# Optimization experiments

Hardware: AMD Instinct MI355X
Metric: run time of the kernel (lower is better)

Reference implementation:

```python
import jax, jax.numpy as jnp
import numpy as np

B, T, C, H = 2, 2048, 1024, 16
HD = C // H  # head dim = 64


def setup_inputs() -> dict:
    key = jax.random.key(0)
    ks = jax.random.split(key, 5)
    s = 1.0 / np.sqrt(C)
    return {
        "x": jax.random.normal(ks[0], (B, T, C), dtype=jnp.float32),
        "W_attn": jax.random.normal(ks[1], (3 * C, C), dtype=jnp.float32) * s,
        "b_attn": jax.random.normal(ks[2], (3 * C,), dtype=jnp.float32) * 0.02,
        "W_proj": jax.random.normal(ks[3], (C, C), dtype=jnp.float32) * s,
        "b_proj": jax.random.normal(ks[4], (C,), dtype=jnp.float32) * 0.02,
    }


def reference(x, W_attn, b_attn, W_proj, b_proj):
    Bx, Tx, Cx = x.shape
    # fused QKV projection (torch Linear: x @ W.T + b)
    qkv = x @ W_attn.T + b_attn                      # [B,T,3C]
    q, k, v = jnp.split(qkv, 3, axis=-1)
    # [B,T,C] -> [B,H,T,hd]
    q = q.reshape(Bx, Tx, H, HD).transpose(0, 2, 1, 3)
    k = k.reshape(Bx, Tx, H, HD).transpose(0, 2, 1, 3)
    v = v.reshape(Bx, Tx, H, HD).transpose(0, 2, 1, 3)
    scale = 1.0 / np.sqrt(HD)
    att = jnp.einsum('bhqd,bhkd->bhqk', q, k) * scale  # [B,H,T,T]
    causal = jnp.tril(jnp.ones((Tx, Tx), dtype=bool))
    att = jnp.where(causal[None, None], att, -jnp.inf)
    att = jax.nn.softmax(att, axis=-1)
    y = jnp.einsum('bhqk,bhkd->bhqd', att, v)          # [B,H,T,hd]
    y = y.transpose(0, 2, 1, 3).reshape(Bx, Tx, Cx)
    return y @ W_proj.T + b_proj
```

## Files before the change

### kernel.cpp

```cpp
#include <hip/hip_runtime.h>

typedef unsigned short ushort_t;
typedef __bf16 bf16x8 __attribute__((ext_vector_type(8)));
typedef float f32x4 __attribute__((ext_vector_type(4)));

__device__ inline ushort_t f2bf(float f) {
  unsigned int u = __builtin_bit_cast(unsigned int, f);
  u += 0x7fff + ((u >> 16) & 1);
  return (ushort_t)(u >> 16);
}

__device__ inline unsigned pk_bf(float a, float b) {
  unsigned ua = __builtin_bit_cast(unsigned, a);
  unsigned ub = __builtin_bit_cast(unsigned, b);
  ua += 0x7fff + ((ua >> 16) & 1);
  ub += 0x7fff + ((ub >> 16) & 1);
  return __builtin_amdgcn_perm(ub, ua, 0x07060302);
}

__device__ inline void async_ld16(const ushort_t* g, const ushort_t* l) {
  __builtin_amdgcn_global_load_lds(
      (const __attribute__((address_space(1))) void*)g,
      (__attribute__((address_space(3))) void*)l, 16, 0, 0);
}

template <int IMM>
__device__ inline void waitcnt_barrier() {
  asm volatile("" ::: "memory");
  __builtin_amdgcn_s_waitcnt(IMM);
  __builtin_amdgcn_s_barrier();
  asm volatile("" ::: "memory");
}

__global__ void cvt_all(const float* __restrict__ x, const float* __restrict__ wa,
                        const float* __restrict__ wp, ushort_t* __restrict__ xb,
                        ushort_t* __restrict__ wab, ushort_t* __restrict__ wpb) {
  int i = blockIdx.x * 256 + threadIdx.x;
  const float* src;
  ushort_t* dst;
  int off;
  if (i < 1048576) { src = x; dst = xb; off = i; }
  else if (i < 1835008) { src = wa; dst = wab; off = i - 1048576; }
  else { src = wp; dst = wpb; off = i - 1835008; }
  float4 f = ((const float4*)src)[off];
  unsigned long long p = (unsigned long long)f2bf(f.x)
      | ((unsigned long long)f2bf(f.y) << 16)
      | ((unsigned long long)f2bf(f.z) << 32)
      | ((unsigned long long)f2bf(f.w) << 48);
  ((unsigned long long*)dst)[off] = p;
}

template <int BM, int BN, int IM, int JN, int MODE>
__global__ __launch_bounds__(256) void gemm_bt(
    const ushort_t* __restrict__ A, const ushort_t* __restrict__ B,
    const float* __restrict__ bias, float* __restrict__ Cf,
    ushort_t* __restrict__ Cb, ushort_t* __restrict__ vtb,
    int M, int N, int K, int ldc, float qscale) {
  constexpr int NWN = BN / (JN * 16);
  constexpr int NL = (BM + BN) / 64;
  constexpr int WIMM = 0x0F70 | NL;
  __shared__ __align__(16) ushort_t As[3][BM * 32];
  __shared__ __align__(16) ushort_t Bs[3][BN * 32];
  const int tid = threadIdx.x;
  const int wave = tid >> 6, lane = tid & 63;
  const int quad = lane >> 4, l16 = lane & 15;
  const int wr = wave / NWN, wc = wave % NWN;
  const int wm = wr * IM * 16, wn = wc * JN * 16;
  const int m0 = blockIdx.y * BM, n0 = blockIdx.x * BN;
  const ushort_t* Ag = A + (size_t)m0 * K;
  const ushort_t* Bg = B + (size_t)n0 * K;
  const int slot = (quad ^ ((l16 >> 1) & 3)) * 8;
  f32x4 acc[IM][JN] = {};

  auto stage = [&](int kt, int bsel) {
    int k0 = kt * 32;
#pragma unroll
    for (int p = 0; p < BM / 64; ++p) {
      int ci = p * 256 + tid;
      int row = ci >> 2, ch = (ci & 3) ^ ((ci >> 3) & 3);
      async_ld16(Ag + (size_t)row * K + k0 + ch * 8, As[bsel] + (p * 256 + wave * 64) * 8);
    }
#pragma unroll
    for (int p = 0; p < BN / 64; ++p) {
      int ci = p * 256 + tid;
      int row = ci >> 2, ch = (ci & 3) ^ ((ci >> 3) & 3);
      async_ld16(Bg + (size_t)row * K + k0 + ch * 8, Bs[bsel] + (p * 256 + wave * 64) * 8);
    }
  };

  const int KT = K / 32;
  stage(0, 0);
  stage(1, 1);
  for (int kt = 0; kt < KT; ++kt) {
    waitcnt_barrier<WIMM>();
    if (kt + 2 < KT) stage(kt + 2, (kt + 2) % 3);
    const ushort_t* Ac = As[kt % 3];
    const ushort_t* Bc = Bs[kt % 3];
    bf16x8 af[IM], bfr[JN];
#pragma unroll
    for (int i = 0; i < IM; ++i)
      af[i] = *(const bf16x8*)(Ac + (wm + i * 16 + l16) * 32 + slot);
#pragma unroll
    for (int j = 0; j < JN; ++j)
      bfr[j] = *(const bf16x8*)(Bc + (wn + j * 16 + l16) * 32 + slot);
#pragma unroll
    for (int i = 0; i < IM; ++i)
#pragma unroll
      for (int j = 0; j < JN; ++j)
        acc[i][j] = __builtin_amdgcn_mfma_f32_16x16x32_bf16(af[i], bfr[j], acc[i][j], 0, 0, 0);
  }

  if (MODE == 1 && n0 >= 2048) {
#pragma unroll
    for (int j = 0; j < JN; ++j) {
      int col = n0 + wn + j * 16 + l16;
      int cv = col - 2048;
      float bv = bias[col];
      size_t rowbase = ((size_t)(cv >> 6)) * 64 + (cv & 63);
#pragma unroll
      for (int i = 0; i < IM; ++i) {
        int rowb = m0 + wm + i * 16 + quad * 4;
        int bb = rowb >> 11, t = rowb & 2047;
        uint2 pp;
        pp.x = pk_bf(acc[i][j][0] + bv, acc[i][j][1] + bv);
        pp.y = pk_bf(acc[i][j][2] + bv, acc[i][j][3] + bv);
        *(uint2*)(vtb + (((size_t)bb * 1024 + rowbase) * 2048 + t)) = pp;
      }
    }
    return;
  }
#pragma unroll
  for (int j = 0; j < JN; ++j) {
    int col = n0 + wn + j * 16 + l16;
    float bv = bias[col];
    float sc = (MODE == 1 && col < 1024) ? qscale : 1.0f;
#pragma unroll
    for (int i = 0; i < IM; ++i)
#pragma unroll
      for (int r = 0; r < 4; ++r) {
        int row = m0 + wm + i * 16 + quad * 4 + r;
        float v = (acc[i][j][r] + bv) * sc;
        if (MODE == 1)
          Cb[(size_t)row * ldc + col] = f2bf(v);
        else
          Cf[(size_t)row * ldc + col] = v;
      }
  }
}

__global__ __launch_bounds__(256) void flash2(
    const ushort_t* __restrict__ qk, const ushort_t* __restrict__ vt,
    ushort_t* __restrict__ y) {
  __shared__ __align__(16) ushort_t Kb[3][4096];
  __shared__ __align__(16) ushort_t Vb[3][4096];
  __shared__ __align__(16) ushort_t Qa[4096], Qb[4096];
  __shared__ __align__(16) ushort_t Ps[64 * 72];
  const int tid = threadIdx.x, wave = tid >> 6, lane = tid & 63;
  const int quad = lane >> 4, l16 = lane & 15;
  const int r7 = l16 & 7;
  const int p = blockIdx.x, bh = blockIdx.y;
  const int b = bh >> 4, h = bh & 15;
  const int bT = b * 2048;
  const int qtA = 31 - p, qtB = p;

  auto stage = [&](int kt, int bsel) {
    int k0 = kt * 64;
#pragma unroll
    for (int i = 0; i < 2; ++i) {
      int ci = i * 256 + tid;
      int row = ci >> 3, ch = (ci & 7) ^ (row & 7);
      async_ld16(qk + (size_t)(bT + k0 + row) * 2048 + 1024 + h * 64 + ch * 8,
                 Kb[bsel] + (i * 256 + wave * 64) * 8);
      async_ld16(vt + (size_t)(bh * 64 + row) * 2048 + k0 + ch * 8,
                 Vb[bsel] + (i * 256 + wave * 64) * 8);
    }
  };

#pragma unroll
  for (int i = 0; i < 2; ++i) {
    int ci = i * 256 + tid;
    int row = ci >> 3, ch = (ci & 7) ^ (row & 7);
    async_ld16(qk + (size_t)(bT + qtA * 64 + row) * 2048 + h * 64 + ch * 8,
               Qa + (i * 256 + wave * 64) * 8);
    async_ld16(qk + (size_t)(bT + qtB * 64 + row) * 2048 + h * 64 + ch * 8,
               Qb + (i * 256 + wave * 64) * 8);
  }
  stage(0, 0);
  stage(1, 1);
  waitcnt_barrier<0x0F78>();
  bf16x8 qaA[2], qaB[2];
#pragma unroll
  for (int ks = 0; ks < 2; ++ks) {
    int off = (wave * 16 + l16) * 64 + (((ks * 4 + quad) ^ r7) * 8);
    qaA[ks] = *(const bf16x8*)(Qa + off);
    qaB[ks] = *(const bf16x8*)(Qb + off);
  }

  f32x4 oA[4] = {}, oB[4] = {};
  float lA = 0.f, lB = 0.f;

  auto process = [&](const bf16x8* qa, f32x4* o, float& l, bool diag,
                     const ushort_t* Kc, const ushort_t* Vc) {
    f32x4 s[4] = {};
#pragma unroll
    for (int ks = 0; ks < 2; ++ks) {
      bf16x8 qf = qa[ks];
#pragma unroll
      for (int j = 0; j < 4; ++j) {
        bf16x8 kf = *(const bf16x8*)(Kc + (j * 16 + l16) * 64 + (((ks * 4 + quad) ^ r7) * 8));
        s[j] = __builtin_amdgcn_mfma_f32_16x16x32_bf16(kf, qf, s[j], 0, 0, 0);
      }
    }
    if (diag) {
      int qloc = wave * 16 + l16;
#pragma unroll
      for (int j = 0; j < 4; ++j)
#pragma unroll
        for (int r = 0; r < 4; ++r)
          if (j * 16 + quad * 4 + r > qloc) s[j][r] = -1e30f;
    }
    float rs = 0.f;
#pragma unroll
    for (int j = 0; j < 4; ++j)
#pragma unroll
      for (int r = 0; r < 4; ++r) {
        float pv = exp2f(s[j][r]);
        s[j][r] = pv;
        rs += pv;
      }
    rs += __shfl_xor(rs, 16, 64);
    rs += __shfl_xor(rs, 32, 64);
    l += rs;
#pragma unroll
    for (int j = 0; j < 4; ++j) {
      uint2 pp;
      pp.x = pk_bf(s[j][0], s[j][1]);
      pp.y = pk_bf(s[j][2], s[j][3]);
      *(uint2*)(Ps + (wave * 16 + l16) * 72 + j * 16 + quad * 4) = pp;
    }
    __builtin_amdgcn_s_waitcnt(0xc07f);
#pragma unroll
    for (int ks = 0; ks < 2; ++ks) {
      bf16x8 pf = *(const bf16x8*)(Ps + (wave * 16 + l16) * 72 + ks * 32 + quad * 8);
#pragma unroll
      for (int j = 0; j < 4; ++j) {
        bf16x8 vf = *(const bf16x8*)(Vc + (j * 16 + l16) * 64 + (((ks * 4 + quad) ^ r7) * 8));
        o[j] = __builtin_amdgcn_mfma_f32_16x16x32_bf16(vf, pf, o[j], 0, 0, 0);
      }
    }
  };

  const int KT = qtA + 1;
  for (int kt = 0; kt < KT; ++kt) {
    waitcnt_barrier<0x0F74>();
    if (kt + 2 < KT) stage(kt + 2, (kt + 2) % 3);
    const ushort_t* Kc = Kb[kt % 3];
    const ushort_t* Vc = Vb[kt % 3];
    process(qaA, oA, lA, kt == qtA, Kc, Vc);
    if (kt <= qtB) process(qaB, oB, lB, kt == qtB, Kc, Vc);
  }

  auto wrt = [&](int qt, f32x4* o, float l) {
    float inv = 1.f / l;
    size_t row = (size_t)(bT + qt * 64 + wave * 16 + l16);
#pragma unroll
    for (int j = 0; j < 4; ++j) {
      uint2 pp;
      pp.x = pk_bf(o[j][0] * inv, o[j][1] * inv);
      pp.y = pk_bf(o[j][2] * inv, o[j][3] * inv);
      *(uint2*)(y + row * 1024 + h * 64 + j * 16 + quad * 4) = pp;
    }
  };
  wrt(qtA, oA, lA);
  wrt(qtB, oB, lB);
}

extern "C" void kernel_launch(void* const* d_in, const int* in_sizes, int n_in,
                              void* d_out, int out_size, void* d_ws, size_t ws_size,
                              hipStream_t stream) {
  const float* x  = (const float*)d_in[0];
  const float* Wa = (const float*)d_in[1];
  const float* ba = (const float*)d_in[2];
  const float* Wp = (const float*)d_in[3];
  const float* bp = (const float*)d_in[4];
  float* out = (float*)d_out;
  char* ws = (char*)d_ws;
  ushort_t* xb  = (ushort_t*)(ws);
  ushort_t* Wab = (ushort_t*)(ws + 8388608);
  ushort_t* Wpb = (ushort_t*)(ws + 14680064);
  ushort_t* qkb = (ushort_t*)(ws + 16777216);
  ushort_t* yb  = (ushort_t*)(ws + 33554432);
  ushort_t* vtb = (ushort_t*)(ws + 41943040);

  cvt_all<<<8192, 256, 0, stream>>>(x, Wa, Wp, xb, Wab, Wpb);
  gemm_bt<128, 128, 4, 4, 1><<<dim3(24, 32), 256, 0, stream>>>(
      xb, Wab, ba, nullptr, qkb, vtb, 4096, 3072, 1024, 2048, 0.18033688011112042f);
  flash2<<<dim3(16, 32), 256, 0, stream>>>(qkb, vtb, yb);
  gemm_bt<64, 64, 2, 2, 0><<<dim3(16, 64), 256, 0, stream>>>(
      yb, Wpb, bp, out, nullptr, nullptr, 4096, 1024, 1024, 1024, 1.0f);
}
```

Before: 202.3 us.

## Replace LDS-staged paired-tile flash attention with direct-load one-tile-per-block kernel

The attention kernel no longer stages K/V tiles through triple-buffered shared memory with barriers. Each wave now loads its K and V fragments straight from global memory into registers, and each block handles one query tile instead of a balanced pair, launching twice as many blocks. The goal is to remove barrier and LDS traffic and raise occupancy through much smaller shared memory use. In exchange, the four waves each reload the same K/V from global or L2, and the causal workload is now unbalanced across blocks.

Result: slower. 377.3 us (+86.5%).

```diff
diff --git a/kernel.cpp b/kernel.cpp
--- a/kernel.cpp
+++ b/kernel.cpp
@@ -148,70 +148,57 @@
   }
 }
 
-__global__ __launch_bounds__(256) void flash2(
+__global__ __launch_bounds__(256) void flash3(
     const ushort_t* __restrict__ qk, const ushort_t* __restrict__ vt,
     ushort_t* __restrict__ y) {
-  __shared__ __align__(16) ushort_t Kb[3][4096];
-  __shared__ __align__(16) ushort_t Vb[3][4096];
-  __shared__ __align__(16) ushort_t Qa[4096], Qb[4096];
-  __shared__ __align__(16) ushort_t Ps[64 * 72];
+  __shared__ __align__(16) ushort_t Ps[4][16 * 72];
   const int tid = threadIdx.x, wave = tid >> 6, lane = tid & 63;
   const int quad = lane >> 4, l16 = lane & 15;
-  const int r7 = l16 & 7;
-  const int p = blockIdx.x, bh = blockIdx.y;
+  const int qt = 31 - blockIdx.x;
+  const int bh = blockIdx.y;
   const int b = bh >> 4, h = bh & 15;
   const int bT = b * 2048;
-  const int qtA = 31 - p, qtB = p;
-
-  auto stage = [&](int kt, int bsel) {
-    int k0 = kt * 64;
-#pragma unroll
-    for (int i = 0; i < 2; ++i) {
-      int ci = i * 256 + tid;
-      int row = ci >> 3, ch = (ci & 7) ^ (row & 7);
-      async_ld16(qk + (size_t)(bT + k0 + row) * 2048 + 1024 + h * 64 + ch * 8,
-                 Kb[bsel] + (i * 256 + wave * 64) * 8);
-      async_ld16(vt + (size_t)(bh * 64 + row) * 2048 + k0 + ch * 8,
-                 Vb[bsel] + (i * 256 + wave * 64) * 8);
-    }
-  };
-
-#pragma unroll
-  for (int i = 0; i < 2; ++i) {
-    int ci = i * 256 + tid;
-    int row = ci >> 3, ch = (ci & 7) ^ (row & 7);
-    async_ld16(qk + (size_t)(bT + qtA * 64 + row) * 2048 + h * 64 + ch * 8,
-               Qa + (i * 256 + wave * 64) * 8);
-    async_ld16(qk + (size_t)(bT + qtB * 64 + row) * 2048 + h * 64 + ch * 8,
-               Qb + (i * 256 + wave * 64) * 8);
-  }
-  stage(0, 0);
-  stage(1, 1);
-  waitcnt_barrier<0x0F78>();
-  bf16x8 qaA[2], qaB[2];
-#pragma unroll
-  for (int ks = 0; ks < 2; ++ks) {
-    int off = (wave * 16 + l16) * 64 + (((ks * 4 + quad) ^ r7) * 8);
-    qaA[ks] = *(const bf16x8*)(Qa + off);
-    qaB[ks] = *(const bf16x8*)(Qb + off);
-  }
-
-  f32x4 oA[4] = {}, oB[4] = {};
-  float lA = 0.f, lB = 0.f;
-
-  auto process = [&](const bf16x8* qa, f32x4* o, float& l, bool diag,
-                     const ushort_t* Kc, const ushort_t* Vc) {
+  const int q0 = qt * 64;
+  ushort_t* Pw = Ps[wave];
+
+  const ushort_t* qrow = qk + (size_t)(bT + q0 + wave * 16 + l16) * 2048 + h * 64 + quad * 8;
+  bf16x8 qf[2];
+  qf[0] = *(const bf16x8*)(qrow);
+  qf[1] = *(const bf16x8*)(qrow + 32);
+
+  const ushort_t* kp[4];
+  const ushort_t* vp[4];
+#pragma unroll
+  for (int j = 0; j < 4; ++j) {
+    kp[j] = qk + (size_t)(bT + j * 16 + l16) * 2048 + 1024 + h * 64 + quad * 8;
+    vp[j] = vt + (size_t)(bh * 64 + j * 16 + l16) * 2048 + quad * 8;
+  }
+
+  f32x4 o[4] = {};
+  float lacc = 0.f;
+
+  for (int kt = 0; kt <= qt; ++kt) {
+    bf16x8 kf[4][2];
+#pragma unroll
+    for (int j = 0; j < 4; ++j) {
+      kf[j][0] = *(const bf16x8*)(kp[j]);
+      kf[j][1] = *(const bf16x8*)(kp[j] + 32);
+    }
     f32x4 s[4] = {};
 #pragma unroll
-    for (int ks = 0; ks < 2; ++ks) {
-      bf16x8 qf = qa[ks];
-#pragma unroll
-      for (int j = 0; j < 4; ++j) {
-        bf16x8 kf = *(const bf16x8*)(Kc + (j * 16 + l16) * 64 + (((ks * 4 + quad) ^ r7) * 8));
-        s[j] = __builtin_amdgcn_mfma_f32_16x16x32_bf16(kf, qf, s[j], 0, 0, 0);
-      }
-    }
-    if (diag) {
+    for (int ks = 0; ks < 2; ++ks)
+#pragma unroll
+      for (int j = 0; j < 4; ++j)
+        s[j] = __builtin_amdgcn_mfma_f32_16x16x32_bf16(kf[j][ks], qf[ks], s[j], 0, 0, 0);
+    bf16x8 vf[4][2];
+#pragma unroll
+    for (int j = 0; j < 4; ++j) {
+      vf[j][0] = *(const bf16x8*)(vp[j]);
+      vf[j][1] = *(const bf16x8*)(vp[j] + 32);
+      kp[j] += 64 * 2048;
+      vp[j] += 64;
+    }
+    if (kt == qt) {
       int qloc = wave * 16 + l16;
 #pragma unroll
       for (int j = 0; j < 4; ++j)
@@ -219,60 +206,43 @@
         for (int r = 0; r < 4; ++r)
           if (j * 16 + quad * 4 + r > qloc) s[j][r] = -1e30f;
     }
-    float rs = 0.f;
 #pragma unroll
     for (int j = 0; j < 4; ++j)
 #pragma unroll
       for (int r = 0; r < 4; ++r) {
         float pv = exp2f(s[j][r]);
         s[j][r] = pv;
-        rs += pv;
+        lacc += pv;
       }
-    rs += __shfl_xor(rs, 16, 64);
-    rs += __shfl_xor(rs, 32, 64);
-    l += rs;
 #pragma unroll
     for (int j = 0; j < 4; ++j) {
       uint2 pp;
       pp.x = pk_bf(s[j][0], s[j][1]);
       pp.y = pk_bf(s[j][2], s[j][3]);
-      *(uint2*)(Ps + (wave * 16 + l16) * 72 + j * 16 + quad * 4) = pp;
+      *(uint2*)(Pw + l16 * 72 + j * 16 + quad * 4) = pp;
     }
     __builtin_amdgcn_s_waitcnt(0xc07f);
-#pragma unroll
-    for (int ks = 0; ks < 2; ++ks) {
-      bf16x8 pf = *(const bf16x8*)(Ps + (wave * 16 + l16) * 72 + ks * 32 + quad * 8);
-#pragma unroll
-      for (int j = 0; j < 4; ++j) {
-        bf16x8 vf = *(const bf16x8*)(Vc + (j * 16 + l16) * 64 + (((ks * 4 + quad) ^ r7) * 8));
-        o[j] = __builtin_amdgcn_mfma_f32_16x16x32_bf16(vf, pf, o[j], 0, 0, 0);
-      }
-    }
-  };
-
-  const int KT = qtA + 1;
-  for (int kt = 0; kt < KT; ++kt) {
-    waitcnt_barrier<0x0F74>();
-    if (kt + 2 < KT) stage(kt + 2, (kt + 2) % 3);
-    const ushort_t* Kc = Kb[kt % 3];
-    const ushort_t* Vc = Vb[kt % 3];
-    process(qaA, oA, lA, kt == qtA, Kc, Vc);
-    if (kt <= qtB) process(qaB, oB, lB, kt == qtB, Kc, Vc);
-  }
-
-  auto wrt = [&](int qt, f32x4* o, float l) {
-    float inv = 1.f / l;
-    size_t row = (size_t)(bT + qt * 64 + wave * 16 + l16);
-#pragma unroll
-    for (int j = 0; j < 4; ++j) {
-      uint2 pp;
-      pp.x = pk_bf(o[j][0] * inv, o[j][1] * inv);
-      pp.y = pk_bf(o[j][2] * inv, o[j][3] * inv);
-      *(uint2*)(y + row * 1024 + h * 64 + j * 16 + quad * 4) = pp;
-    }
-  };
-  wrt(qtA, oA, lA);
-  wrt(qtB, oB, lB);
+    bf16x8 pf[2];
+    pf[0] = *(const bf16x8*)(Pw + l16 * 72 + quad * 8);
+    pf[1] = *(const bf16x8*)(Pw + l16 * 72 + 32 + quad * 8);
+#pragma unroll
+    for (int ks = 0; ks < 2; ++ks)
+#pragma unroll
+      for (int j = 0; j < 4; ++j)
+        o[j] = __builtin_amdgcn_mfma_f32_16x16x32_bf16(vf[j][ks], pf[ks], o[j], 0, 0, 0);
+  }
+
+  lacc += __shfl_xor(lacc, 16, 64);
+  lacc += __shfl_xor(lacc, 32, 64);
+  float inv = 1.f / lacc;
+  size_t row = (size_t)(bT + q0 + wave * 16 + l16);
+#pragma unroll
+  for (int j = 0; j < 4; ++j) {
+    uint2 pp;
+    pp.x = pk_bf(o[j][0] * inv, o[j][1] * inv);
+    pp.y = pk_bf(o[j][2] * inv, o[j][3] * inv);
+    *(uint2*)(y + row * 1024 + h * 64 + j * 16 + quad * 4) = pp;
+  }
 }
 
 extern "C" void kernel_launch(void* const* d_in, const int* in_sizes, int n_in,
@@ -295,7 +265,7 @@
   cvt_all<<<8192, 256, 0, stream>>>(x, Wa, Wp, xb, Wab, Wpb);
   gemm_bt<128, 128, 4, 4, 1><<<dim3(24, 32), 256, 0, stream>>>(
       xb, Wab, ba, nullptr, qkb, vtb, 4096, 3072, 1024, 2048, 0.18033688011112042f);
-  flash2<<<dim3(16, 32), 256, 0, stream>>>(qkb, vtb, yb);
+  flash3<<<dim3(32, 32), 256, 0, stream>>>(qkb, vtb, yb);
   gemm_bt<64, 64, 2, 2, 0><<<dim3(16, 64), 256, 0, stream>>>(
       yb, Wpb, bp, out, nullptr, nullptr, 4096, 1024, 1024, 1024, 1.0f);
 }
```

## Use 8-wave QKV GEMM and interleave two query tiles in flash kernel

Applied to the files above, without the earlier changes.

The QKV GEMM becomes a 512-thread, 8-wave kernel with each wave holding a 4x2 tile instead of 4x4, and the staging loops are generalized to the thread count. The flash kernel loads K fragments once per step and reuses them for both query tiles, gives each tile its own per-wave P buffer, and interleaves the two tiles' MFMAs. It also defers the cross-lane row-sum reduction to the final write. The aim is more latency hiding and fewer redundant LDS reads, at the cost of higher register pressure and possible occupancy loss.

New measurement: 239.2 us. 1.18x slower.

```diff
diff --git a/kernel.cpp b/kernel.cpp
--- a/kernel.cpp
+++ b/kernel.cpp
@@ -50,14 +50,14 @@
   ((unsigned long long*)dst)[off] = p;
 }
 
-template <int BM, int BN, int IM, int JN, int MODE>
-__global__ __launch_bounds__(256) void gemm_bt(
+template <int BM, int BN, int IM, int JN, int MODE, int TPB>
+__global__ __launch_bounds__(TPB) void gemm_bt(
     const ushort_t* __restrict__ A, const ushort_t* __restrict__ B,
     const float* __restrict__ bias, float* __restrict__ Cf,
     ushort_t* __restrict__ Cb, ushort_t* __restrict__ vtb,
     int M, int N, int K, int ldc, float qscale) {
   constexpr int NWN = BN / (JN * 16);
-  constexpr int NL = (BM + BN) / 64;
+  constexpr int NL = (BM + BN) * 32 / (TPB * 8);
   constexpr int WIMM = 0x0F70 | NL;
   __shared__ __align__(16) ushort_t As[3][BM * 32];
   __shared__ __align__(16) ushort_t Bs[3][BN * 32];
@@ -75,16 +75,16 @@
   auto stage = [&](int kt, int bsel) {
     int k0 = kt * 32;
 #pragma unroll
-    for (int p = 0; p < BM / 64; ++p) {
-      int ci = p * 256 + tid;
+    for (int p = 0; p < BM * 4 / TPB; ++p) {
+      int ci = p * TPB + tid;
       int row = ci >> 2, ch = (ci & 3) ^ ((ci >> 3) & 3);
-      async_ld16(Ag + (size_t)row * K + k0 + ch * 8, As[bsel] + (p * 256 + wave * 64) * 8);
-    }
-#pragma unroll
-    for (int p = 0; p < BN / 64; ++p) {
-      int ci = p * 256 + tid;
+      async_ld16(Ag + (size_t)row * K + k0 + ch * 8, As[bsel] + (p * TPB + wave * 64) * 8);
+    }
+#pragma unroll
+    for (int p = 0; p < BN * 4 / TPB; ++p) {
+      int ci = p * TPB + tid;
       int row = ci >> 2, ch = (ci & 3) ^ ((ci >> 3) & 3);
-      async_ld16(Bg + (size_t)row * K + k0 + ch * 8, Bs[bsel] + (p * 256 + wave * 64) * 8);
+      async_ld16(Bg + (size_t)row * K + k0 + ch * 8, Bs[bsel] + (p * TPB + wave * 64) * 8);
     }
   };
 
@@ -148,13 +148,13 @@
   }
 }
 
-__global__ __launch_bounds__(256) void flash2(
+__global__ __launch_bounds__(256) void flash4(
     const ushort_t* __restrict__ qk, const ushort_t* __restrict__ vt,
     ushort_t* __restrict__ y) {
   __shared__ __align__(16) ushort_t Kb[3][4096];
   __shared__ __align__(16) ushort_t Vb[3][4096];
   __shared__ __align__(16) ushort_t Qa[4096], Qb[4096];
-  __shared__ __align__(16) ushort_t Ps[64 * 72];
+  __shared__ __align__(16) ushort_t Ps[8][16 * 72];
   const int tid = threadIdx.x, wave = tid >> 6, lane = tid & 63;
   const int quad = lane >> 4, l16 = lane & 15;
   const int r7 = l16 & 7;
@@ -162,6 +162,8 @@
   const int b = bh >> 4, h = bh & 15;
   const int bT = b * 2048;
   const int qtA = 31 - p, qtB = p;
+  ushort_t* PwA = Ps[wave];
+  ushort_t* PwB = Ps[wave + 4];
 
   auto stage = [&](int kt, int bsel) {
     int k0 = kt * 64;
@@ -188,67 +190,16 @@
   stage(0, 0);
   stage(1, 1);
   waitcnt_barrier<0x0F78>();
-  bf16x8 qaA[2], qaB[2];
+  bf16x8 qfA[2], qfB[2];
 #pragma unroll
   for (int ks = 0; ks < 2; ++ks) {
     int off = (wave * 16 + l16) * 64 + (((ks * 4 + quad) ^ r7) * 8);
-    qaA[ks] = *(const bf16x8*)(Qa + off);
-    qaB[ks] = *(const bf16x8*)(Qb + off);
+    qfA[ks] = *(const bf16x8*)(Qa + off);
+    qfB[ks] = *(const bf16x8*)(Qb + off);
   }
 
   f32x4 oA[4] = {}, oB[4] = {};
   float lA = 0.f, lB = 0.f;
-
-  auto process = [&](const bf16x8* qa, f32x4* o, float& l, bool diag,
-                     const ushort_t* Kc, const ushort_t* Vc) {
-    f32x4 s[4] = {};
-#pragma unroll
-    for (int ks = 0; ks < 2; ++ks) {
-      bf16x8 qf = qa[ks];
-#pragma unroll
-      for (int j = 0; j < 4; ++j) {
-        bf16x8 kf = *(const bf16x8*)(Kc + (j * 16 + l16) * 64 + (((ks * 4 + quad) ^ r7) * 8));
-        s[j] = __builtin_amdgcn_mfma_f32_16x16x32_bf16(kf, qf, s[j], 0, 0, 0);
-      }
-    }
-    if (diag) {
-      int qloc = wave * 16 + l16;
-#pragma unroll
-      for (int j = 0; j < 4; ++j)
-#pragma unroll
-        for (int r = 0; r < 4; ++r)
-          if (j * 16 + quad * 4 + r > qloc) s[j][r] = -1e30f;
-    }
-    float rs = 0.f;
-#pragma unroll
-    for (int j = 0; j < 4; ++j)
-#pragma unroll
-      for (int r = 0; r < 4; ++r) {
-        float pv = exp2f(s[j][r]);
-        s[j][r] = pv;
-        rs += pv;
-      }
-    rs += __shfl_xor(rs, 16, 64);
-    rs += __shfl_xor(rs, 32, 64);
-    l += rs;
-#pragma unroll
-    for (int j = 0; j < 4; ++j) {
-      uint2 pp;
-      pp.x = pk_bf(s[j][0], s[j][1]);
-      pp.y = pk_bf(s[j][2], s[j][3]);
-      *(uint2*)(Ps + (wave * 16 + l16) * 72 + j * 16 + quad * 4) = pp;
-    }
-    __builtin_amdgcn_s_waitcnt(0xc07f);
-#pragma unroll
-    for (int ks = 0; ks < 2; ++ks) {
-      bf16x8 pf = *(const bf16x8*)(Ps + (wave * 16 + l16) * 72 + ks * 32 + quad * 8);
-#pragma unroll
-      for (int j = 0; j < 4; ++j) {
-        bf16x8 vf = *(const bf16x8*)(Vc + (j * 16 + l16) * 64 + (((ks * 4 + quad) ^ r7) * 8));
-        o[j] = __builtin_amdgcn_mfma_f32_16x16x32_bf16(vf, pf, o[j], 0, 0, 0);
-      }
-    }
-  };
 
   const int KT = qtA + 1;
   for (int kt = 0; kt < KT; ++kt) {
@@ -256,11 +207,87 @@
     if (kt + 2 < KT) stage(kt + 2, (kt + 2) % 3);
     const ushort_t* Kc = Kb[kt % 3];
     const ushort_t* Vc = Vb[kt % 3];
-    process(qaA, oA, lA, kt == qtA, Kc, Vc);
-    if (kt <= qtB) process(qaB, oB, lB, kt == qtB, Kc, Vc);
+    const bool doB = (kt <= qtB);
+
+    bf16x8 kf[4][2];
+#pragma unroll
+    for (int j = 0; j < 4; ++j)
+#pragma unroll
+      for (int ks = 0; ks < 2; ++ks)
+        kf[j][ks] = *(const bf16x8*)(Kc + (j * 16 + l16) * 64 + (((ks * 4 + quad) ^ r7) * 8));
+    f32x4 sA[4] = {}, sB[4] = {};
+#pragma unroll
+    for (int ks = 0; ks < 2; ++ks)
+#pragma unroll
+      for (int j = 0; j < 4; ++j)
+        sA[j] = __builtin_amdgcn_mfma_f32_16x16x32_bf16(kf[j][ks], qfA[ks], sA[j], 0, 0, 0);
+    if (doB)
+#pragma unroll
+      for (int ks = 0; ks < 2; ++ks)
+#pragma unroll
+        for (int j = 0; j < 4; ++j)
+          sB[j] = __builtin_amdgcn_mfma_f32_16x16x32_bf16(kf[j][ks], qfB[ks], sB[j], 0, 0, 0);
+    int qloc = wave * 16 + l16;
+    if (kt == qtA)
+#pragma unroll
+      for (int j = 0; j < 4; ++j)
+#pragma unroll
+        for (int r = 0; r < 4; ++r)
+          if (j * 16 + quad * 4 + r > qloc) sA[j][r] = -1e30f;
+    if (kt == qtB)
+#pragma unroll
+      for (int j = 0; j < 4; ++j)
+#pragma unroll
+        for (int r = 0; r < 4; ++r)
+          if (j * 16 + quad * 4 + r > qloc) sB[j][r] = -1e30f;
+#pragma unroll
+    for (int j = 0; j < 4; ++j) {
+#pragma unroll
+      for (int r = 0; r < 4; ++r) {
+        float pv = exp2f(sA[j][r]);
+        sA[j][r] = pv;
+        lA += pv;
+      }
+      uint2 pp;
+      pp.x = pk_bf(sA[j][0], sA[j][1]);
+      pp.y = pk_bf(sA[j][2], sA[j][3]);
+      *(uint2*)(PwA + l16 * 72 + j * 16 + quad * 4) = pp;
+    }
+    if (doB)
+#pragma unroll
+      for (int j = 0; j < 4; ++j) {
+#pragma unroll
+        for (int r = 0; r < 4; ++r) {
+          float pv = exp2f(sB[j][r]);
+          sB[j][r] = pv;
+          lB += pv;
+        }
+        uint2 pp;
+        pp.x = pk_bf(sB[j][0], sB[j][1]);
+        pp.y = pk_bf(sB[j][2], sB[j][3]);
+        *(uint2*)(PwB + l16 * 72 + j * 16 + quad * 4) = pp;
+      }
+    __builtin_amdgcn_s_waitcnt(0xc07f);
+    bf16x8 pfA[2], pfB[2];
+#pragma unroll
+    for (int ks = 0; ks < 2; ++ks) {
+      pfA[ks] = *(const bf16x8*)(PwA + l16 * 72 + ks * 32 + quad * 8);
+      pfB[ks] = *(const bf16x8*)(PwB + l16 * 72 + ks * 32 + quad * 8);
+    }
+#pragma unroll
+    for (int ks = 0; ks < 2; ++ks)
+#pragma unroll
+      for (int j = 0; j < 4; ++j) {
+        bf16x8 vf = *(const bf16x8*)(Vc + (j * 16 + l16) * 64 + (((ks * 4 + quad) ^ r7) * 8));
+        oA[j] = __builtin_amdgcn_mfma_f32_16x16x32_bf16(vf, pfA[ks], oA[j], 0, 0, 0);
+        if (doB)
+          oB[j] = __builtin_amdgcn_mfma_f32_16x16x32_bf16(vf, pfB[ks], oB[j], 0, 0, 0);
+      }
   }
 
   auto wrt = [&](int qt, f32x4* o, float l) {
+    l += __shfl_xor(l, 16, 64);
+    l += __shfl_xor(l, 32, 64);
     float inv = 1.f / l;
     size_t row = (size_t)(bT + qt * 64 + wave * 16 + l16);
 #pragma unroll
@@ -293,9 +320,9 @@
   ushort_t* vtb = (ushort_t*)(ws + 41943040);
 
   cvt_all<<<8192, 256, 0, stream>>>(x, Wa, Wp, xb, Wab, Wpb);
-  gemm_bt<128, 128, 4, 4, 1><<<dim3(24, 32), 256, 0, stream>>>(
+  gemm_bt<128, 128, 4, 2, 1, 512><<<dim3(24, 32), 512, 0, stream>>>(
       xb, Wab, ba, nullptr, qkb, vtb, 4096, 3072, 1024, 2048, 0.18033688011112042f);
-  flash2<<<dim3(16, 32), 256, 0, stream>>>(qkb, vtb, yb);
-  gemm_bt<64, 64, 2, 2, 0><<<dim3(16, 64), 256, 0, stream>>>(
+  flash4<<<dim3(16, 32), 256, 0, stream>>>(qkb, vtb, yb);
+  gemm_bt<64, 64, 2, 2, 0, 256><<<dim3(16, 64), 256, 0, stream>>>(
       yb, Wpb, bp, out, nullptr, nullptr, 4096, 1024, 1024, 1024, 1.0f);
 }
```
